# Performance work log

Measured on AMD Instinct MI355X. Metric: run time of the kernel, lower is better.

## Reference

```python
import jax, jax.numpy as jnp
import numpy as np

N_PROP = 1000
N_CLS = 81  # includes background class 0
IMG_H, IMG_W = 800, 1333
WX, WY, WW, WH = 10.0, 10.0, 5.0, 5.0
BBOX_XFORM_CLIP = float(np.log(1000.0 / 16.0))
SCORE_THRESH = 0.05
NMS_THRESH = 0.5
DET_PER_IMG = 100


def _decode(box_regression, proposals):
    widths = proposals[:, 2] - proposals[:, 0] + 1.0
    heights = proposals[:, 3] - proposals[:, 1] + 1.0
    ctr_x = proposals[:, 0] + 0.5 * widths
    ctr_y = proposals[:, 1] + 0.5 * heights
    rel = box_regression.reshape(box_regression.shape[0], -1, 4)  # [N, C, 4]
    dx = rel[..., 0] / WX
    dy = rel[..., 1] / WY
    dw = jnp.minimum(rel[..., 2] / WW, BBOX_XFORM_CLIP)
    dh = jnp.minimum(rel[..., 3] / WH, BBOX_XFORM_CLIP)
    pcx = dx * widths[:, None] + ctr_x[:, None]
    pcy = dy * heights[:, None] + ctr_y[:, None]
    pw = jnp.exp(dw) * widths[:, None]
    ph = jnp.exp(dh) * heights[:, None]
    return jnp.stack([pcx - 0.5 * pw, pcy - 0.5 * ph,
                      pcx + 0.5 * pw - 1.0, pcy + 0.5 * ph - 1.0], axis=-1)  # [N, C, 4]


def _clip_boxes(b, h, w):
    x1 = jnp.clip(b[..., 0], 0.0, w - 1.0)
    y1 = jnp.clip(b[..., 1], 0.0, h - 1.0)
    x2 = jnp.clip(b[..., 2], 0.0, w - 1.0)
    y2 = jnp.clip(b[..., 3], 0.0, h - 1.0)
    return jnp.stack([x1, y1, x2, y2], axis=-1)


def _nms_keep(boxes, scores, valid):
    # Greedy NMS for one class. boxes [N,4], scores [N], valid [N].
    # Returns keep mask in the ORIGINAL proposal order.
    n = scores.shape[0]
    order = jnp.argsort(-jnp.where(valid, scores, -jnp.inf))
    b = boxes[order]
    v = valid[order]
    x1, y1, x2, y2 = b[:, 0], b[:, 1], b[:, 2], b[:, 3]
    area = (x2 - x1 + 1.0) * (y2 - y1 + 1.0)
    iw = jnp.clip(jnp.minimum(x2[:, None], x2[None, :]) - jnp.maximum(x1[:, None], x1[None, :]) + 1.0, 0.0)
    ih = jnp.clip(jnp.minimum(y2[:, None], y2[None, :]) - jnp.maximum(y1[:, None], y1[None, :]) + 1.0, 0.0)
    inter = iw * ih
    iou = inter / (area[:, None] + area[None, :] - inter)
    idx = jnp.arange(n)

    def body(i, keep):
        sup = (iou[i] > NMS_THRESH) & (idx > i) & keep[i]
        return keep & ~sup

    keep = jax.lax.fori_loop(0, n, body, v)
    return jnp.zeros(n, dtype=bool).at[order].set(keep)


def _postprocess(class_logits, box_regression, proposal_boxes, image_h, image_w):
    prob = jax.nn.softmax(class_logits, axis=-1)             # [N, C]
    boxes = _decode(box_regression, proposal_boxes)           # [N, C, 4]
    boxes = _clip_boxes(boxes, float(image_h), float(image_w))
    scores_c = prob[:, 1:].T                                  # [C-1, N] skip background
    boxes_c = jnp.transpose(boxes[:, 1:, :], (1, 0, 2))       # [C-1, N, 4]
    valid = scores_c > SCORE_THRESH
    keep = jax.vmap(_nms_keep)(boxes_c, scores_c, valid)      # [C-1, N]
    masked = jnp.where(keep, scores_c, -jnp.inf)
    count = jnp.sum(keep)
    # torch.kthvalue(n - 100) == 101st largest kept score; keep scores >= it
    topv = jax.lax.top_k(masked.reshape(-1), DET_PER_IMG + 1)[0]
    image_thresh = jnp.where(count > DET_PER_IMG, topv[DET_PER_IMG], -jnp.inf)
    final = keep & (masked >= image_thresh)
    c1, n = scores_c.shape
    labels = jnp.broadcast_to(jnp.arange(1, c1 + 1, dtype=jnp.int32)[:, None], (c1, n))
    out_scores = jnp.where(final, scores_c, 0.0).reshape(-1)
    out_boxes = jnp.where(final[..., None], boxes_c, 0.0).reshape(-1, 4)
    out5 = jnp.concatenate([out_boxes, out_scores[:, None]], axis=1)  # [(C-1)*N, 5]
    return out5, jnp.where(final, labels, 0).reshape(-1), final.reshape(-1)


def setup_inputs() -> dict:
    key = jax.random.key(0)
    k1, k2, k3, k4 = jax.random.split(key, 4)
    # scale logits so a realistic fraction of softmax scores clears the 0.05 threshold
    class_logits = 3.0 * jax.random.normal(k1, (N_PROP, N_CLS), dtype=jnp.float32)
    box_regression = jax.random.normal(k2, (N_PROP, N_CLS * 4), dtype=jnp.float32)
    cxy = jax.random.uniform(k3, (N_PROP, 2), dtype=jnp.float32) * jnp.array([IMG_W, IMG_H], jnp.float32)
    wh = 16.0 + 284.0 * jax.random.uniform(k4, (N_PROP, 2), dtype=jnp.float32)
    x1y1 = jnp.clip(cxy - 0.5 * wh, 0.0)
    x2y2 = jnp.minimum(cxy + 0.5 * wh, jnp.array([IMG_W - 1.0, IMG_H - 1.0], jnp.float32))
    proposal_boxes = jnp.concatenate([x1y1, x2y2], axis=1)  # [N, 4] xyxy
    return {"class_logits": class_logits, "box_regression": box_regression,
            "proposal_boxes": proposal_boxes, "image_h": IMG_H, "image_w": IMG_W}


def reference(class_logits, box_regression, proposal_boxes, image_h, image_w):
    return _postprocess(class_logits, box_regression, proposal_boxes, image_h, image_w)
```

## Files before the change

kernel.cpp:

```cpp
#include <hip/hip_runtime.h>
#include <math.h>

#define N_PROP 1000
#define N_CLS  81
#define N_FG   80
#define SCORE_THRESH 0.05f
#define NMS_THRESH   0.5f
#define DET_PER_IMG  100
#define BBOX_CLIP    4.135166556742356f

#define LBL_OFF    400000
#define FIN_OFF    480000


__global__ __launch_bounds__(256)
void softmax_zero_kernel(const float* __restrict__ logits,
                         float* __restrict__ out,
                         int* __restrict__ count,
                         int* __restrict__ done,
                         float* __restrict__ probT) {
    const int b = blockIdx.x;
    const int t = threadIdx.x;
    const int lane = t & 63;
    const int wave = t >> 6;
    if (b == 0 && t == 0) { *count = 0; *done = 0; }

    float4 z = make_float4(0.f, 0.f, 0.f, 0.f);
    float4* o4 = (float4*)out;
    for (int i = b * 256 + t; i < 140000; i += 250 * 256) o4[i] = z;

    const int n = b * 4 + wave;
    if (n < N_PROP) {
        const float* lrow = logits + (size_t)n * N_CLS;
        float v0 = lrow[lane];
        float v1 = (lane + 64 < N_CLS) ? lrow[lane + 64] : -INFINITY;
        float m = fmaxf(v0, v1);
        for (int off = 32; off; off >>= 1) m = fmaxf(m, __shfl_down(m, off));
        m = __shfl(m, 0);
        float e0 = expf(v0 - m);
        float e1 = (lane + 64 < N_CLS) ? expf(v1 - m) : 0.0f;
        float s = e0 + e1;
        for (int off = 32; off; off >>= 1) s += __shfl_down(s, off);
        s = __shfl(s, 0);
        if (lane >= 1)          probT[(size_t)(lane - 1) * N_PROP + n] = e0 / s;
        if (lane + 64 < N_CLS)  probT[(size_t)(lane + 63) * N_PROP + n] = e1 / s;
    }
}

__global__ __launch_bounds__(256)
void nms_kernel(const float* __restrict__ probT,
                const float* __restrict__ props,
                const float* __restrict__ reg,
                const int* __restrict__ ihp,
                const int* __restrict__ iwp,
                float* __restrict__ out,
                int* __restrict__ count,
                int* __restrict__ done,
                float* __restrict__ compact,
                int* __restrict__ svRow) {
    const int c = blockIdx.x;
    const int t = threadIdx.x;
    const int lane = t & 63;
    const int wave = t >> 6;
    const int cls = c + 1;

    __shared__ float sSc[N_PROP];
    __shared__ int   sIdx[N_PROP];
    __shared__ int   sPos[N_PROP];
    __shared__ float sx1[N_PROP], sy1[N_PROP], sx2[N_PROP], sy2[N_PROP];
    __shared__ float sar[N_PROP], sSc2[N_PROP];
    __shared__ int   sJdx[N_PROP];
    __shared__ unsigned char sKeep[N_PROP];
    __shared__ unsigned long long smask[512][8];
    __shared__ unsigned long long skeepW[8];
    __shared__ int   shV;
    __shared__ int   sLast;
    __shared__ int   red4[4];

    for (int j = t; j < N_PROP; j += 256) sSc[j] = probT[(size_t)c * N_PROP + j];
    __syncthreads();

    if (wave == 0) {
        int V = 0;
        #pragma unroll
        for (int it = 0; it < 16; ++it) {
            int j = it * 64 + lane;
            float sc = (j < N_PROP) ? sSc[j] : -1.0f;
            bool val = (j < N_PROP) && (sc > SCORE_THRESH);
            unsigned long long mask = __ballot(val);
            int pre = __popcll(mask & ((1ULL << lane) - 1ULL));
            if (val) { sSc[V + pre] = sc; sIdx[V + pre] = j; }
            V += __popcll(mask);
        }
        if (lane == 0) shV = V;
    }
    __syncthreads();
    const int V = shV;

    for (int v = t; v < V; v += 256) {
        float s = sSc[v];
        int id = sIdx[v];
        int r = 0;
        for (int u = 0; u < V; ++u) {
            float su = sSc[u];
            r += (su > s) || (su == s && sIdx[u] < id);
        }
        sPos[v] = r;
    }
    __syncthreads();

    const float W1 = (float)iwp[0] - 1.0f;
    const float H1 = (float)ihp[0] - 1.0f;
    for (int v = t; v < V; v += 256) {
        int r = sPos[v];
        int j = sIdx[v];
        float4 pr = *(const float4*)(props + (size_t)j * 4);
        float w  = pr.z - pr.x + 1.0f;
        float h  = pr.w - pr.y + 1.0f;
        float cx = pr.x + 0.5f * w;
        float cy = pr.y + 0.5f * h;
        float4 rr = *(const float4*)(reg + ((size_t)j * N_CLS + cls) * 4);
        float dx = rr.x / 10.0f;
        float dy = rr.y / 10.0f;
        float dw = fminf(rr.z / 5.0f, BBOX_CLIP);
        float dh = fminf(rr.w / 5.0f, BBOX_CLIP);
        float pcx = dx * w + cx;
        float pcy = dy * h + cy;
        float pw = expf(dw) * w;
        float ph = expf(dh) * h;
        float bx1 = pcx - 0.5f * pw;
        float by1 = pcy - 0.5f * ph;
        float bx2 = pcx + 0.5f * pw - 1.0f;
        float by2 = pcy + 0.5f * ph - 1.0f;
        bx1 = fminf(fmaxf(bx1, 0.0f), W1);
        bx2 = fminf(fmaxf(bx2, 0.0f), W1);
        by1 = fminf(fmaxf(by1, 0.0f), H1);
        by2 = fminf(fmaxf(by2, 0.0f), H1);
        sx1[r] = bx1; sy1[r] = by1; sx2[r] = bx2; sy2[r] = by2;
        sar[r] = (bx2 - bx1 + 1.0f) * (by2 - by1 + 1.0f);
        sSc2[r] = sSc[v];
        sJdx[r] = j;
        sKeep[r] = 1;
    }
    __syncthreads();

    if (V <= 512) {
        const int nW = (V + 63) >> 6;
        for (int r = t; r < V; r += 256) {
            const float X1 = sx1[r], Y1 = sy1[r], X2 = sx2[r], Y2 = sy2[r], A = sar[r];
            for (int w = 0; w < nW; ++w) {
                unsigned long long bits = 0ull;
                int v0 = w << 6;
                int vs = (r + 1 > v0) ? r + 1 : v0;
                int ve = (V < v0 + 64) ? V : v0 + 64;
                for (int v = vs; v < ve; ++v) {
                    float iw = fminf(X2, sx2[v]) - fmaxf(X1, sx1[v]) + 1.0f;
                    float ih = fminf(Y2, sy2[v]) - fmaxf(Y1, sy1[v]) + 1.0f;
                    iw = fmaxf(iw, 0.0f);
                    ih = fmaxf(ih, 0.0f);
                    float inter = iw * ih;
                    float iou = inter / (A + sar[v] - inter);
                    if (iou > NMS_THRESH) bits |= 1ull << (v - v0);
                }
                smask[r][w] = bits;
            }
        }
        __syncthreads();

        if (t == 0) {
            for (int w = 0; w < 8; ++w) {
                int rem = V - (w << 6);
                skeepW[w] = (rem >= 64) ? ~0ull : (rem <= 0 ? 0ull : ((1ull << rem) - 1ull));
            }
            for (int r = 0; r < V; ++r) {
                if ((skeepW[r >> 6] >> (r & 63)) & 1ull) {
                    for (int w = r >> 6; w < (int)((V + 63) >> 6); ++w) skeepW[w] &= ~smask[r][w];
                }
            }
        }
        __syncthreads();
        for (int v = t; v < V; v += 256)
            sKeep[v] = (unsigned char)((skeepW[v >> 6] >> (v & 63)) & 1ull);
        __syncthreads();
    } else {
        for (int r = 0; r < V; ++r) {
            if (sKeep[r]) {
                const float X1 = sx1[r], Y1 = sy1[r], X2 = sx2[r], Y2 = sy2[r], A = sar[r];
                for (int v = r + 1 + t; v < V; v += 256) {
                    if (sKeep[v]) {
                        float iw = fminf(X2, sx2[v]) - fmaxf(X1, sx1[v]) + 1.0f;
                        float ih = fminf(Y2, sy2[v]) - fmaxf(Y1, sy1[v]) + 1.0f;
                        iw = fmaxf(iw, 0.0f);
                        ih = fmaxf(ih, 0.0f);
                        float inter = iw * ih;
                        float iou = inter / (A + sar[v] - inter);
                        if (iou > NMS_THRESH) sKeep[v] = 0;
                    }
                }
            }
            __syncthreads();
        }
    }

    for (int v = t; v < V; v += 256) {
        if (sKeep[v]) {
            int row = c * N_PROP + sJdx[v];
            size_t o = (size_t)row * 5;
            out[o + 0] = sx1[v];
            out[o + 1] = sy1[v];
            out[o + 2] = sx2[v];
            out[o + 3] = sy2[v];
            out[o + 4] = sSc2[v];
            out[LBL_OFF + row] = (float)cls;
            out[FIN_OFF + row] = 1.0f;
            int pos = atomicAdd(count, 1);
            compact[pos] = sSc2[v];
            svRow[pos] = row;
        }
    }
    __syncthreads();

    __threadfence();
    if (t == 0) {
        int old = __hip_atomic_fetch_add(done, 1, __ATOMIC_ACQ_REL, __HIP_MEMORY_SCOPE_AGENT);
        sLast = (old == N_FG - 1) ? 1 : 0;
    }
    __syncthreads();
    if (!sLast) return;
    __threadfence();

    const int n = __hip_atomic_load(count, __ATOMIC_RELAXED, __HIP_MEMORY_SCOPE_AGENT);
    float* lsc = (float*)smask;

    float th = 0.0f;
    const bool useL = (n <= 8192);
    if (n > DET_PER_IMG) {
        if (useL) {
            for (int i = t; i < n; i += 256)
                lsc[i] = __hip_atomic_load(&compact[i], __ATOMIC_RELAXED, __HIP_MEMORY_SCOPE_AGENT);
            __syncthreads();
        }
        unsigned lo = 0x3D4CCCCCu, hi = 0x40000000u;
        while (hi - lo > 1u) {
            unsigned mid = lo + ((hi - lo) >> 1);
            float mv = __uint_as_float(mid);
            int cnt = 0;
            if (useL) {
                for (int i = t; i < n; i += 256) cnt += (lsc[i] >= mv) ? 1 : 0;
            } else {
                for (int i = t; i < n; i += 256)
                    cnt += (__hip_atomic_load(&compact[i], __ATOMIC_RELAXED, __HIP_MEMORY_SCOPE_AGENT) >= mv) ? 1 : 0;
            }
            for (int off = 32; off; off >>= 1) cnt += __shfl_down(cnt, off);
            if (lane == 0) red4[wave] = cnt;
            __syncthreads();
            int total = red4[0] + red4[1] + red4[2] + red4[3];
            __syncthreads();
            if (total >= DET_PER_IMG + 1) lo = mid; else hi = mid;
        }
        th = __uint_as_float(lo);
    }

    for (int i = t; i < n; i += 256) {
        float sc = useL ? lsc[i]
                        : __hip_atomic_load(&compact[i], __ATOMIC_RELAXED, __HIP_MEMORY_SCOPE_AGENT);
        if (sc < th) {
            int row = __hip_atomic_load(&svRow[i], __ATOMIC_RELAXED, __HIP_MEMORY_SCOPE_AGENT);
            size_t o = (size_t)row * 5;
            out[o + 0] = 0.0f;
            out[o + 1] = 0.0f;
            out[o + 2] = 0.0f;
            out[o + 3] = 0.0f;
            out[o + 4] = 0.0f;
            out[LBL_OFF + row] = 0.0f;
            out[FIN_OFF + row] = 0.0f;
        }
    }
}

extern "C" void kernel_launch(void* const* d_in, const int* in_sizes, int n_in,
                              void* d_out, int out_size, void* d_ws, size_t ws_size,
                              hipStream_t stream) {
    const float* logits = (const float*)d_in[0];
    const float* reg    = (const float*)d_in[1];
    const float* props  = (const float*)d_in[2];
    const int*   ihp    = (const int*)d_in[3];
    const int*   iwp    = (const int*)d_in[4];
    float* out = (float*)d_out;

    char* ws = (char*)d_ws;
    int*   count   = (int*)(ws + 0);
    int*   done    = (int*)(ws + 4);
    float* probT   = (float*)(ws + 64);
    float* compact = (float*)(ws + 320064);
    int*   svRow   = (int*)(ws + 640064);

    softmax_zero_kernel<<<250, 256, 0, stream>>>(logits, out, count, done, probT);
    nms_kernel<<<N_FG, 256, 0, stream>>>(probT, props, reg, ihp, iwp,
                                         out, count, done, compact, svRow);
}
```

Baseline: 74.51 us.

## Rewrite per-class NMS as single-wavefront register-resident greedy suppression

```diff
diff --git a/kernel.cpp b/kernel.cpp
--- a/kernel.cpp
+++ b/kernel.cpp
@@ -47,7 +47,33 @@
     }
 }
 
-__global__ __launch_bounds__(256)
+__device__ __forceinline__ void decode_box(const float* __restrict__ props,
+                                           const float* __restrict__ reg,
+                                           int j, int cls, float W1, float H1,
+                                           float& bx1, float& by1, float& bx2,
+                                           float& by2, float& area) {
+    float4 pr = *(const float4*)(props + (size_t)j * 4);
+    float w  = pr.z - pr.x + 1.0f;
+    float h  = pr.w - pr.y + 1.0f;
+    float cx = pr.x + 0.5f * w;
+    float cy = pr.y + 0.5f * h;
+    float4 rr = *(const float4*)(reg + ((size_t)j * N_CLS + cls) * 4);
+    float dx = rr.x / 10.0f;
+    float dy = rr.y / 10.0f;
+    float dw = fminf(rr.z / 5.0f, BBOX_CLIP);
+    float dh = fminf(rr.w / 5.0f, BBOX_CLIP);
+    float pcx = dx * w + cx;
+    float pcy = dy * h + cy;
+    float pw = expf(dw) * w;
+    float ph = expf(dh) * h;
+    bx1 = fminf(fmaxf(pcx - 0.5f * pw, 0.0f), W1);
+    by1 = fminf(fmaxf(pcy - 0.5f * ph, 0.0f), H1);
+    bx2 = fminf(fmaxf(pcx + 0.5f * pw - 1.0f, 0.0f), W1);
+    by2 = fminf(fmaxf(pcy + 0.5f * ph - 1.0f, 0.0f), H1);
+    area = (bx2 - bx1 + 1.0f) * (by2 - by1 + 1.0f);
+}
+
+__global__ __launch_bounds__(64)
 void nms_kernel(const float* __restrict__ probT,
                 const float* __restrict__ props,
                 const float* __restrict__ reg,
@@ -59,219 +85,200 @@
                 float* __restrict__ compact,
                 int* __restrict__ svRow) {
     const int c = blockIdx.x;
-    const int t = threadIdx.x;
-    const int lane = t & 63;
-    const int wave = t >> 6;
+    const int lane = threadIdx.x;
     const int cls = c + 1;
-
-    __shared__ float sSc[N_PROP];
-    __shared__ int   sIdx[N_PROP];
-    __shared__ int   sPos[N_PROP];
-    __shared__ float sx1[N_PROP], sy1[N_PROP], sx2[N_PROP], sy2[N_PROP];
-    __shared__ float sar[N_PROP], sSc2[N_PROP];
-    __shared__ int   sJdx[N_PROP];
-    __shared__ unsigned char sKeep[N_PROP];
-    __shared__ unsigned long long smask[512][8];
-    __shared__ unsigned long long skeepW[8];
-    __shared__ int   shV;
-    __shared__ int   sLast;
-    __shared__ int   red4[4];
-
-    for (int j = t; j < N_PROP; j += 256) sSc[j] = probT[(size_t)c * N_PROP + j];
-    __syncthreads();
-
-    if (wave == 0) {
-        int V = 0;
-        #pragma unroll
-        for (int it = 0; it < 16; ++it) {
-            int j = it * 64 + lane;
-            float sc = (j < N_PROP) ? sSc[j] : -1.0f;
-            bool val = (j < N_PROP) && (sc > SCORE_THRESH);
-            unsigned long long mask = __ballot(val);
-            int pre = __popcll(mask & ((1ULL << lane) - 1ULL));
-            if (val) { sSc[V + pre] = sc; sIdx[V + pre] = j; }
-            V += __popcll(mask);
-        }
-        if (lane == 0) shV = V;
-    }
-    __syncthreads();
-    const int V = shV;
-
-    for (int v = t; v < V; v += 256) {
-        float s = sSc[v];
-        int id = sIdx[v];
-        int r = 0;
-        for (int u = 0; u < V; ++u) {
-            float su = sSc[u];
-            r += (su > s) || (su == s && sIdx[u] < id);
-        }
-        sPos[v] = r;
-    }
-    __syncthreads();
+    const unsigned long long lmask = (1ull << lane) - 1ull;
+
+    __shared__ float2 sComp[N_PROP];
+    __shared__ float2 sSort[128];
+    __shared__ float  sF[8192];
 
     const float W1 = (float)iwp[0] - 1.0f;
     const float H1 = (float)ihp[0] - 1.0f;
-    for (int v = t; v < V; v += 256) {
-        int r = sPos[v];
-        int j = sIdx[v];
-        float4 pr = *(const float4*)(props + (size_t)j * 4);
-        float w  = pr.z - pr.x + 1.0f;
-        float h  = pr.w - pr.y + 1.0f;
-        float cx = pr.x + 0.5f * w;
-        float cy = pr.y + 0.5f * h;
-        float4 rr = *(const float4*)(reg + ((size_t)j * N_CLS + cls) * 4);
-        float dx = rr.x / 10.0f;
-        float dy = rr.y / 10.0f;
-        float dw = fminf(rr.z / 5.0f, BBOX_CLIP);
-        float dh = fminf(rr.w / 5.0f, BBOX_CLIP);
-        float pcx = dx * w + cx;
-        float pcy = dy * h + cy;
-        float pw = expf(dw) * w;
-        float ph = expf(dh) * h;
-        float bx1 = pcx - 0.5f * pw;
-        float by1 = pcy - 0.5f * ph;
-        float bx2 = pcx + 0.5f * pw - 1.0f;
-        float by2 = pcy + 0.5f * ph - 1.0f;
-        bx1 = fminf(fmaxf(bx1, 0.0f), W1);
-        bx2 = fminf(fmaxf(bx2, 0.0f), W1);
-        by1 = fminf(fmaxf(by1, 0.0f), H1);
-        by2 = fminf(fmaxf(by2, 0.0f), H1);
-        sx1[r] = bx1; sy1[r] = by1; sx2[r] = bx2; sy2[r] = by2;
-        sar[r] = (bx2 - bx1 + 1.0f) * (by2 - by1 + 1.0f);
-        sSc2[r] = sSc[v];
-        sJdx[r] = j;
-        sKeep[r] = 1;
+
+    float scv[16];
+    #pragma unroll
+    for (int it = 0; it < 16; ++it) {
+        int j = it * 64 + lane;
+        scv[it] = (j < N_PROP) ? probT[(size_t)c * N_PROP + j] : -1.0f;
+    }
+    int V = 0;
+    #pragma unroll
+    for (int it = 0; it < 16; ++it) {
+        int j = it * 64 + lane;
+        bool val = (j < N_PROP) && (scv[it] > SCORE_THRESH);
+        unsigned long long mask = __ballot(val);
+        if (val) sComp[V + __popcll(mask & lmask)] = make_float2(scv[it], __int_as_float(j));
+        V += __popcll(mask);
     }
     __syncthreads();
 
-    if (V <= 512) {
-        const int nW = (V + 63) >> 6;
-        for (int r = t; r < V; r += 256) {
-            const float X1 = sx1[r], Y1 = sy1[r], X2 = sx2[r], Y2 = sy2[r], A = sar[r];
-            for (int w = 0; w < nW; ++w) {
-                unsigned long long bits = 0ull;
-                int v0 = w << 6;
-                int vs = (r + 1 > v0) ? r + 1 : v0;
-                int ve = (V < v0 + 64) ? V : v0 + 64;
-                for (int v = vs; v < ve; ++v) {
-                    float iw = fminf(X2, sx2[v]) - fmaxf(X1, sx1[v]) + 1.0f;
-                    float ih = fminf(Y2, sy2[v]) - fmaxf(Y1, sy1[v]) + 1.0f;
-                    iw = fmaxf(iw, 0.0f);
-                    ih = fmaxf(ih, 0.0f);
-                    float inter = iw * ih;
-                    float iou = inter / (A + sar[v] - inter);
-                    if (iou > NMS_THRESH) bits |= 1ull << (v - v0);
-                }
-                smask[r][w] = bits;
-            }
-        }
+    if (V <= 128) {
+        float s0 = -1.0f, s1 = -1.0f; int i0 = 0, i1 = 0;
+        if (lane < V)      { float2 q = sComp[lane];      s0 = q.x; i0 = __float_as_int(q.y); }
+        if (64 + lane < V) { float2 q = sComp[64 + lane]; s1 = q.x; i1 = __float_as_int(q.y); }
+
+        int r0 = 0, r1 = 0;
+        for (int u = 0; u < V; ++u) {
+            float2 q = sComp[u];
+            float su = q.x; int iu = __float_as_int(q.y);
+            r0 += (su > s0) || (su == s0 && iu < i0);
+            r1 += (su > s1) || (su == s1 && iu < i1);
+        }
+        if (lane < V)      sSort[r0] = make_float2(s0, __int_as_float(i0));
+        if (64 + lane < V) sSort[r1] = make_float2(s1, __int_as_float(i1));
         __syncthreads();
 
-        if (t == 0) {
-            for (int w = 0; w < 8; ++w) {
-                int rem = V - (w << 6);
-                skeepW[w] = (rem >= 64) ? ~0ull : (rem <= 0 ? 0ull : ((1ull << rem) - 1ull));
-            }
-            for (int r = 0; r < V; ++r) {
-                if ((skeepW[r >> 6] >> (r & 63)) & 1ull) {
-                    for (int w = r >> 6; w < (int)((V + 63) >> 6); ++w) skeepW[w] &= ~smask[r][w];
-                }
-            }
+        float sc0 = 0.f, sc1 = 0.f; int j0 = 0, j1 = 0;
+        if (lane < V)      { float2 q = sSort[lane];      sc0 = q.x; j0 = __float_as_int(q.y); }
+        if (64 + lane < V) { float2 q = sSort[64 + lane]; sc1 = q.x; j1 = __float_as_int(q.y); }
+
+        float x10, y10, x20, y20, a0, x11, y11, x21, y21, a1;
+        decode_box(props, reg, j0, cls, W1, H1, x10, y10, x20, y20, a0);
+        decode_box(props, reg, j1, cls, W1, H1, x11, y11, x21, y21, a1);
+
+        bool al0 = (lane < V), al1 = (64 + lane < V);
+        unsigned long long am0 = __ballot(al0), am1 = __ballot(al1);
+        for (int r = 0; r < V; ++r) {
+            bool aliveR = (r < 64) ? ((am0 >> r) & 1ull) : ((am1 >> (r - 64)) & 1ull);
+            if (!aliveR) continue;
+            float X1, Y1, X2, Y2, A;
+            if (r < 64) {
+                X1 = __shfl(x10, r); Y1 = __shfl(y10, r);
+                X2 = __shfl(x20, r); Y2 = __shfl(y20, r); A = __shfl(a0, r);
+            } else {
+                X1 = __shfl(x11, r - 64); Y1 = __shfl(y11, r - 64);
+                X2 = __shfl(x21, r - 64); Y2 = __shfl(y21, r - 64); A = __shfl(a1, r - 64);
+            }
+            if (al0 && lane > r) {
+                float iw = fmaxf(fminf(X2, x20) - fmaxf(X1, x10) + 1.0f, 0.0f);
+                float ih = fmaxf(fminf(Y2, y20) - fmaxf(Y1, y10) + 1.0f, 0.0f);
+                float inter = iw * ih;
+                float iou = inter / (A + a0 - inter);
+                if (iou > NMS_THRESH) al0 = false;
+            }
+            if (al1 && 64 + lane > r) {
+                float iw = fmaxf(fminf(X2, x21) - fmaxf(X1, x11) + 1.0f, 0.0f);
+                float ih = fmaxf(fminf(Y2, y21) - fmaxf(Y1, y11) + 1.0f, 0.0f);
+                float inter = iw * ih;
+                float iou = inter / (A + a1 - inter);
+                if (iou > NMS_THRESH) al1 = false;
+            }
+            am0 = __ballot(al0); am1 = __ballot(al1);
+        }
+
+        int n0 = __popcll(am0), n1 = __popcll(am1);
+        int base = 0;
+        if (lane == 0 && (n0 + n1) > 0) base = atomicAdd(count, n0 + n1);
+        base = __shfl(base, 0);
+        if (al0) {
+            int row = c * N_PROP + j0;
+            size_t o = (size_t)row * 5;
+            out[o + 0] = x10; out[o + 1] = y10; out[o + 2] = x20; out[o + 3] = y20; out[o + 4] = sc0;
+            out[LBL_OFF + row] = (float)cls;
+            out[FIN_OFF + row] = 1.0f;
+            int pos = base + __popcll(am0 & lmask);
+            compact[pos] = sc0; svRow[pos] = row;
+        }
+        if (al1) {
+            int row = c * N_PROP + j1;
+            size_t o = (size_t)row * 5;
+            out[o + 0] = x11; out[o + 1] = y11; out[o + 2] = x21; out[o + 3] = y21; out[o + 4] = sc1;
+            out[LBL_OFF + row] = (float)cls;
+            out[FIN_OFF + row] = 1.0f;
+            int pos = base + n0 + __popcll(am1 & lmask);
+            compact[pos] = sc1; svRow[pos] = row;
+        }
+    } else {
+        float* fx1 = sF;          float* fy1 = sF + 1000;
+        float* fx2 = sF + 2000;   float* fy2 = sF + 3000;
+        float* fa  = sF + 4000;   float* fs  = sF + 5000;
+        int*   fj  = (int*)(sF + 6000);
+        int*   fk  = (int*)(sF + 7000);
+        for (int v = lane; v < V; v += 64) {
+            float2 q = sComp[v];
+            float s = q.x; int id = __float_as_int(q.y);
+            int r = 0;
+            for (int u = 0; u < V; ++u) {
+                float2 qu = sComp[u];
+                r += (qu.x > s) || (qu.x == s && __float_as_int(qu.y) < id);
+            }
+            float bx1, by1, bx2, by2, ar;
+            decode_box(props, reg, id, cls, W1, H1, bx1, by1, bx2, by2, ar);
+            fx1[r] = bx1; fy1[r] = by1; fx2[r] = bx2; fy2[r] = by2;
+            fa[r] = ar; fs[r] = s; fj[r] = id; fk[r] = 1;
         }
         __syncthreads();
-        for (int v = t; v < V; v += 256)
-            sKeep[v] = (unsigned char)((skeepW[v >> 6] >> (v & 63)) & 1ull);
-        __syncthreads();
-    } else {
         for (int r = 0; r < V; ++r) {
-            if (sKeep[r]) {
-                const float X1 = sx1[r], Y1 = sy1[r], X2 = sx2[r], Y2 = sy2[r], A = sar[r];
-                for (int v = r + 1 + t; v < V; v += 256) {
-                    if (sKeep[v]) {
-                        float iw = fminf(X2, sx2[v]) - fmaxf(X1, sx1[v]) + 1.0f;
-                        float ih = fminf(Y2, sy2[v]) - fmaxf(Y1, sy1[v]) + 1.0f;
-                        iw = fmaxf(iw, 0.0f);
-                        ih = fmaxf(ih, 0.0f);
+            if (fk[r]) {
+                const float X1 = fx1[r], Y1 = fy1[r], X2 = fx2[r], Y2 = fy2[r], A = fa[r];
+                for (int v = r + 1 + lane; v < V; v += 64) {
+                    if (fk[v]) {
+                        float iw = fmaxf(fminf(X2, fx2[v]) - fmaxf(X1, fx1[v]) + 1.0f, 0.0f);
+                        float ih = fmaxf(fminf(Y2, fy2[v]) - fmaxf(Y1, fy1[v]) + 1.0f, 0.0f);
                         float inter = iw * ih;
-                        float iou = inter / (A + sar[v] - inter);
-                        if (iou > NMS_THRESH) sKeep[v] = 0;
+                        float iou = inter / (A + fa[v] - inter);
+                        if (iou > NMS_THRESH) fk[v] = 0;
                     }
                 }
             }
             __syncthreads();
         }
-    }
-
-    for (int v = t; v < V; v += 256) {
-        if (sKeep[v]) {
-            int row = c * N_PROP + sJdx[v];
-            size_t o = (size_t)row * 5;
-            out[o + 0] = sx1[v];
-            out[o + 1] = sy1[v];
-            out[o + 2] = sx2[v];
-            out[o + 3] = sy2[v];
-            out[o + 4] = sSc2[v];
-            out[LBL_OFF + row] = (float)cls;
-            out[FIN_OFF + row] = 1.0f;
-            int pos = atomicAdd(count, 1);
-            compact[pos] = sSc2[v];
-            svRow[pos] = row;
-        }
-    }
-    __syncthreads();
+        for (int v = lane; v < V; v += 64) {
+            if (fk[v]) {
+                int row = c * N_PROP + fj[v];
+                size_t o = (size_t)row * 5;
+                out[o + 0] = fx1[v]; out[o + 1] = fy1[v]; out[o + 2] = fx2[v];
+                out[o + 3] = fy2[v]; out[o + 4] = fs[v];
+                out[LBL_OFF + row] = (float)cls;
+                out[FIN_OFF + row] = 1.0f;
+                int pos = atomicAdd(count, 1);
+                compact[pos] = fs[v]; svRow[pos] = row;
+            }
+        }
+        __syncthreads();
+    }
 
     __threadfence();
-    if (t == 0) {
-        int old = __hip_atomic_fetch_add(done, 1, __ATOMIC_ACQ_REL, __HIP_MEMORY_SCOPE_AGENT);
-        sLast = (old == N_FG - 1) ? 1 : 0;
-    }
-    __syncthreads();
-    if (!sLast) return;
+    int old = 0;
+    if (lane == 0) old = __hip_atomic_fetch_add(done, 1, __ATOMIC_ACQ_REL, __HIP_MEMORY_SCOPE_AGENT);
+    old = __shfl(old, 0);
+    if (old != N_FG - 1) return;
     __threadfence();
 
     const int n = __hip_atomic_load(count, __ATOMIC_RELAXED, __HIP_MEMORY_SCOPE_AGENT);
-    float* lsc = (float*)smask;
-
-    float th = 0.0f;
+    if (n <= DET_PER_IMG) return;
+
     const bool useL = (n <= 8192);
-    if (n > DET_PER_IMG) {
+    if (useL) {
+        for (int i = lane; i < n; i += 64)
+            sF[i] = __hip_atomic_load(&compact[i], __ATOMIC_RELAXED, __HIP_MEMORY_SCOPE_AGENT);
+        __syncthreads();
+    }
+    unsigned lo = 0x3D4CCCCCu, hi = 0x40000000u;
+    while (hi - lo > 1u) {
+        unsigned mid = lo + ((hi - lo) >> 1);
+        float mv = __uint_as_float(mid);
+        int cnt = 0;
         if (useL) {
-            for (int i = t; i < n; i += 256)
-                lsc[i] = __hip_atomic_load(&compact[i], __ATOMIC_RELAXED, __HIP_MEMORY_SCOPE_AGENT);
-            __syncthreads();
-        }
-        unsigned lo = 0x3D4CCCCCu, hi = 0x40000000u;
-        while (hi - lo > 1u) {
-            unsigned mid = lo + ((hi - lo) >> 1);
-            float mv = __uint_as_float(mid);
-            int cnt = 0;
-            if (useL) {
-                for (int i = t; i < n; i += 256) cnt += (lsc[i] >= mv) ? 1 : 0;
-            } else {
-                for (int i = t; i < n; i += 256)
-                    cnt += (__hip_atomic_load(&compact[i], __ATOMIC_RELAXED, __HIP_MEMORY_SCOPE_AGENT) >= mv) ? 1 : 0;
-            }
-            for (int off = 32; off; off >>= 1) cnt += __shfl_down(cnt, off);
-            if (lane == 0) red4[wave] = cnt;
-            __syncthreads();
-            int total = red4[0] + red4[1] + red4[2] + red4[3];
-            __syncthreads();
-            if (total >= DET_PER_IMG + 1) lo = mid; else hi = mid;
-        }
-        th = __uint_as_float(lo);
-    }
-
-    for (int i = t; i < n; i += 256) {
-        float sc = useL ? lsc[i]
+            for (int i = lane; i < n; i += 64) cnt += (sF[i] >= mv) ? 1 : 0;
+        } else {
+            for (int i = lane; i < n; i += 64)
+                cnt += (__hip_atomic_load(&compact[i], __ATOMIC_RELAXED, __HIP_MEMORY_SCOPE_AGENT) >= mv) ? 1 : 0;
+        }
+        for (int off = 32; off; off >>= 1) cnt += __shfl_xor(cnt, off);
+        if (cnt >= DET_PER_IMG + 1) lo = mid; else hi = mid;
+    }
+    const float th = __uint_as_float(lo);
+
+    for (int i = lane; i < n; i += 64) {
+        float sc = useL ? sF[i]
                         : __hip_atomic_load(&compact[i], __ATOMIC_RELAXED, __HIP_MEMORY_SCOPE_AGENT);
         if (sc < th) {
             int row = __hip_atomic_load(&svRow[i], __ATOMIC_RELAXED, __HIP_MEMORY_SCOPE_AGENT);
             size_t o = (size_t)row * 5;
-            out[o + 0] = 0.0f;
-            out[o + 1] = 0.0f;
-            out[o + 2] = 0.0f;
-            out[o + 3] = 0.0f;
-            out[o + 4] = 0.0f;
+            out[o + 0] = 0.0f; out[o + 1] = 0.0f; out[o + 2] = 0.0f;
+            out[o + 3] = 0.0f; out[o + 4] = 0.0f;
             out[LBL_OFF + row] = 0.0f;
             out[FIN_OFF + row] = 0.0f;
         }
@@ -296,6 +303,6 @@
     int*   svRow   = (int*)(ws + 640064);
 
     softmax_zero_kernel<<<250, 256, 0, stream>>>(logits, out, count, done, probT);
-    nms_kernel<<<N_FG, 256, 0, stream>>>(probT, props, reg, ihp, iwp,
-                                         out, count, done, compact, svRow);
+    nms_kernel<<<N_FG, 64, 0, stream>>>(probT, props, reg, ihp, iwp,
+                                        out, count, done, compact, svRow);
 }
```

Result: slower. 101.9 us (+36.8%).
